# Optimization experiments

Hardware: AMD Instinct MI355X
Metric: run time of the kernel (lower is better)

Reference implementation:

```python
import jax, jax.numpy as jnp
import numpy as np

BIAS = 0.1  # init kwarg `bias`
B = 8192


def setup_inputs() -> dict:
    key = jax.random.key(0)
    k1, k2, k3 = jax.random.split(key, 3)
    predictions = jax.random.normal(k1, (B,), dtype=jnp.float32)
    correct_output = jax.random.normal(k2, (B,), dtype=jnp.float32)
    weight = jax.random.uniform(k3, (B,), dtype=jnp.float32)
    return {"predictions": predictions, "correct_output": correct_output, "weight": weight}


def reference(predictions, correct_output, weight):
    # pairwise diffs: [B, B], diff[m, n] = pred_m - pred_n
    diff = predictions[:, None] - predictions[None, :]
    gt_diff = correct_output[:, None] - correct_output[None, :]
    # r = +1 if pred_m > pred_n, -1 if pred_m < pred_n, else -sign(gt_m - gt_n)
    r = jnp.where(diff > 0, 1.0, jnp.where(diff < 0, -1.0, -jnp.sign(gt_diff)))
    # weighted by average pair weight
    r = r * (weight[:, None] + weight[None, :]) * 0.5
    loss = jnp.maximum(0.0, BIAS - r * diff)  # hinge per pair
    return jnp.sum(loss) / (B * B)
```

## Files before the change

### kernel.cpp

```cpp
#include <hip/hip_runtime.h>


#define BIAS_F 0.1f

typedef float v2f __attribute__((ext_vector_type(2)));

constexpr int TPB = 512;
constexpr int NPT = 8;
constexpr int NG  = NPT / 2;
constexpr int TN  = TPB * NPT;
constexpr int TM  = 32;

__global__ __launch_bounds__(TPB) void pair_loss_kernel(
    const float* __restrict__ pred,
    const float* __restrict__ weight,
    float* __restrict__ partial,
    int B)
{
    const int n_base = blockIdx.x * TN;
    const int m_base = blockIdx.y * TM;
    const int t = threadIdx.x;

    v2f pn2[NG], wn2[NG], mask2[NG];

    if (n_base + TN <= B) {
        const float4* p4 = reinterpret_cast<const float4*>(pred   + n_base) + 2 * t;
        const float4* w4 = reinterpret_cast<const float4*>(weight + n_base) + 2 * t;
        float4 pa = p4[0], pb = p4[1];
        float4 wa = w4[0], wb = w4[1];
        pn2[0] = (v2f){pa.x, pa.y}; pn2[1] = (v2f){pa.z, pa.w};
        pn2[2] = (v2f){pb.x, pb.y}; pn2[3] = (v2f){pb.z, pb.w};
        wn2[0] = (v2f){wa.x, wa.y} * 0.5f; wn2[1] = (v2f){wa.z, wa.w} * 0.5f;
        wn2[2] = (v2f){wb.x, wb.y} * 0.5f; wn2[3] = (v2f){wb.z, wb.w} * 0.5f;
        #pragma unroll
        for (int j = 0; j < NG; ++j) mask2[j] = (v2f){1.0f, 1.0f};
    } else {
        #pragma unroll
        for (int j = 0; j < NG; ++j) {
            #pragma unroll
            for (int e = 0; e < 2; ++e) {
                int n = n_base + 8 * t + 2 * j + e;
                bool ok = (n < B);
                int nc = ok ? n : 0;
                pn2[j][e]   = pred[nc];
                wn2[j][e]   = weight[nc] * 0.5f;
                mask2[j][e] = ok ? 1.0f : 0.0f;
            }
        }
    }

    v2f acc2[NG];
    #pragma unroll
    for (int j = 0; j < NG; ++j) acc2[j] = (v2f){0.0f, 0.0f};

    const v2f BIAS2 = (v2f){BIAS_F, BIAS_F};
    const int m_end = (m_base + TM <= B) ? TM : (B - m_base);

    #pragma unroll 4
    for (int i = 0; i < m_end; ++i) {
        const int m = m_base + i;
        const float pm  = pred[m];
        const float wmh = weight[m] * 0.5f;
        const v2f pm2 = (v2f){pm, pm};
        const v2f wm2 = (v2f){wmh, wmh};
        #pragma unroll
        for (int j = 0; j < NG; ++j) {
            v2f d  = pm2 - pn2[j];
            v2f w  = wm2 + wn2[j];
            v2f t1 = __builtin_elementwise_fma(-w, d, BIAS2);
            v2f t2 = __builtin_elementwise_fma( w, d, BIAS2);
            v2f h;
            h.x = __builtin_amdgcn_fmed3f(t1.x, t2.x, 0.0f);
            h.y = __builtin_amdgcn_fmed3f(t1.y, t2.y, 0.0f);
            acc2[j] += h;
        }
    }

    float s = 0.0f;
    #pragma unroll
    for (int j = 0; j < NG; ++j)
        s += mask2[j].x * acc2[j].x + mask2[j].y * acc2[j].y;

    #pragma unroll
    for (int off = 32; off > 0; off >>= 1)
        s += __shfl_down(s, off, 64);

    __shared__ float lds[TPB / 64];
    const int lane = t & 63, wid = t >> 6;
    if (lane == 0) lds[wid] = s;
    __syncthreads();
    if (t == 0) {
        float bs = 0.0f;
        #pragma unroll
        for (int w = 0; w < TPB / 64; ++w) bs += lds[w];
        partial[blockIdx.y * gridDim.x + blockIdx.x] = bs;
    }
}

__global__ __launch_bounds__(64) void reduce_kernel(
    const float* __restrict__ partial, int n, float* __restrict__ out, int B)
{
    double s = 0.0;
    for (int i = (int)threadIdx.x; i < n; i += 64) s += (double)partial[i];
    #pragma unroll
    for (int off = 32; off > 0; off >>= 1)
        s += __shfl_down(s, off, 64);
    if (threadIdx.x == 0)
        out[0] = (float)(s / ((double)B * (double)B));
}

extern "C" void kernel_launch(void* const* d_in, const int* in_sizes, int n_in,
                              void* d_out, int out_size, void* d_ws, size_t ws_size,
                              hipStream_t stream) {
    const float* pred   = (const float*)d_in[0];
    const float* weight = (const float*)d_in[2];
    float* out = (float*)d_out;
    const int B = in_sizes[0];

    const int tilesN = (B + TN - 1) / TN;
    const int tilesM = (B + TM - 1) / TM;
    float* partial = (float*)d_ws;

    dim3 grid(tilesN, tilesM);
    pair_loss_kernel<<<grid, TPB, 0, stream>>>(pred, weight, partial, B);
    reduce_kernel<<<1, 64, 0, stream>>>(partial, tilesN * tilesM, out, B);
}
```

Measured before the change: 18.02 us.

## Fuse final reduction into main kernel via fixed-point atomic last-block detection

Removes the separate reduce kernel. Each block now adds its partial sum as a fixed-point value packed with a completion counter into a single 64-bit atomic, and the last block writes the final result. Blocks are restructured to 1024 threads, each looping over all n tiles for its 32-row m tile, so the grid is one-dimensional. A memset launch replaces the reduce launch, and fixed-point quantization and a 48-bit range limit the precision of the sum.

```diff
diff --git a/kernel.cpp b/kernel.cpp
--- a/kernel.cpp
+++ b/kernel.cpp
@@ -2,85 +2,90 @@
 
 
 #define BIAS_F 0.1f
+#define FIX_SCALE 4194304.0
 
 typedef float v2f __attribute__((ext_vector_type(2)));
 
-constexpr int TPB = 512;
+constexpr int TPB = 1024;
 constexpr int NPT = 8;
 constexpr int NG  = NPT / 2;
-constexpr int TN  = TPB * NPT;
+constexpr int TNF = TPB * NPT;
 constexpr int TM  = 32;
 
 __global__ __launch_bounds__(TPB) void pair_loss_kernel(
     const float* __restrict__ pred,
     const float* __restrict__ weight,
-    float* __restrict__ partial,
-    int B)
+    unsigned long long* __restrict__ acc,
+    float* __restrict__ out,
+    int B, int nBlocks)
 {
-    const int n_base = blockIdx.x * TN;
-    const int m_base = blockIdx.y * TM;
+    const int m_base = blockIdx.x * TM;
     const int t = threadIdx.x;
 
-    v2f pn2[NG], wn2[NG], mask2[NG];
+    float s_thread = 0.0f;
+    const v2f BIAS2 = (v2f){BIAS_F, BIAS_F};
 
-    if (n_base + TN <= B) {
-        const float4* p4 = reinterpret_cast<const float4*>(pred   + n_base) + 2 * t;
-        const float4* w4 = reinterpret_cast<const float4*>(weight + n_base) + 2 * t;
-        float4 pa = p4[0], pb = p4[1];
-        float4 wa = w4[0], wb = w4[1];
-        pn2[0] = (v2f){pa.x, pa.y}; pn2[1] = (v2f){pa.z, pa.w};
-        pn2[2] = (v2f){pb.x, pb.y}; pn2[3] = (v2f){pb.z, pb.w};
-        wn2[0] = (v2f){wa.x, wa.y} * 0.5f; wn2[1] = (v2f){wa.z, wa.w} * 0.5f;
-        wn2[2] = (v2f){wb.x, wb.y} * 0.5f; wn2[3] = (v2f){wb.z, wb.w} * 0.5f;
-        #pragma unroll
-        for (int j = 0; j < NG; ++j) mask2[j] = (v2f){1.0f, 1.0f};
-    } else {
-        #pragma unroll
-        for (int j = 0; j < NG; ++j) {
+    for (int n_base = 0; n_base < B; n_base += TNF) {
+        v2f pn2[NG], wn2[NG], mask2[NG];
+        const int n_first = n_base + 8 * t;
+
+        if (n_base + TNF <= B) {
+            const float4* p4 = reinterpret_cast<const float4*>(pred   + n_base) + 2 * t;
+            const float4* w4 = reinterpret_cast<const float4*>(weight + n_base) + 2 * t;
+            float4 pa = p4[0], pb = p4[1];
+            float4 wa = w4[0], wb = w4[1];
+            pn2[0] = (v2f){pa.x, pa.y}; pn2[1] = (v2f){pa.z, pa.w};
+            pn2[2] = (v2f){pb.x, pb.y}; pn2[3] = (v2f){pb.z, pb.w};
+            wn2[0] = (v2f){wa.x, wa.y} * 0.5f; wn2[1] = (v2f){wa.z, wa.w} * 0.5f;
+            wn2[2] = (v2f){wb.x, wb.y} * 0.5f; wn2[3] = (v2f){wb.z, wb.w} * 0.5f;
             #pragma unroll
-            for (int e = 0; e < 2; ++e) {
-                int n = n_base + 8 * t + 2 * j + e;
-                bool ok = (n < B);
-                int nc = ok ? n : 0;
-                pn2[j][e]   = pred[nc];
-                wn2[j][e]   = weight[nc] * 0.5f;
-                mask2[j][e] = ok ? 1.0f : 0.0f;
+            for (int j = 0; j < NG; ++j) mask2[j] = (v2f){1.0f, 1.0f};
+        } else {
+            #pragma unroll
+            for (int j = 0; j < NG; ++j) {
+                #pragma unroll
+                for (int e = 0; e < 2; ++e) {
+                    int n = n_first + 2 * j + e;
+                    bool ok = (n < B);
+                    int nc = ok ? n : 0;
+                    pn2[j][e]   = pred[nc];
+                    wn2[j][e]   = weight[nc] * 0.5f;
+                    mask2[j][e] = ok ? 1.0f : 0.0f;
+                }
             }
         }
+
+        v2f acc2[NG];
+        #pragma unroll
+        for (int j = 0; j < NG; ++j) acc2[j] = (v2f){0.0f, 0.0f};
+
+        const int m_end = (m_base + TM <= B) ? TM : (B - m_base);
+        #pragma unroll 4
+        for (int i = 0; i < m_end; ++i) {
+            const int m = m_base + i;
+            const float pm  = pred[m];
+            const float wmh = weight[m] * 0.5f;
+            const v2f pm2 = (v2f){pm, pm};
+            const v2f wm2 = (v2f){wmh, wmh};
+            #pragma unroll
+            for (int j = 0; j < NG; ++j) {
+                v2f d  = pm2 - pn2[j];
+                v2f w  = wm2 + wn2[j];
+                v2f t1 = __builtin_elementwise_fma(-w, d, BIAS2);
+                v2f t2 = __builtin_elementwise_fma( w, d, BIAS2);
+                v2f h;
+                h.x = __builtin_amdgcn_fmed3f(t1.x, t2.x, 0.0f);
+                h.y = __builtin_amdgcn_fmed3f(t1.y, t2.y, 0.0f);
+                acc2[j] += h;
+            }
+        }
+
+        #pragma unroll
+        for (int j = 0; j < NG; ++j)
+            s_thread += mask2[j].x * acc2[j].x + mask2[j].y * acc2[j].y;
     }
 
-    v2f acc2[NG];
-    #pragma unroll
-    for (int j = 0; j < NG; ++j) acc2[j] = (v2f){0.0f, 0.0f};
-
-    const v2f BIAS2 = (v2f){BIAS_F, BIAS_F};
-    const int m_end = (m_base + TM <= B) ? TM : (B - m_base);
-
-    #pragma unroll 4
-    for (int i = 0; i < m_end; ++i) {
-        const int m = m_base + i;
-        const float pm  = pred[m];
-        const float wmh = weight[m] * 0.5f;
-        const v2f pm2 = (v2f){pm, pm};
-        const v2f wm2 = (v2f){wmh, wmh};
-        #pragma unroll
-        for (int j = 0; j < NG; ++j) {
-            v2f d  = pm2 - pn2[j];
-            v2f w  = wm2 + wn2[j];
-            v2f t1 = __builtin_elementwise_fma(-w, d, BIAS2);
-            v2f t2 = __builtin_elementwise_fma( w, d, BIAS2);
-            v2f h;
-            h.x = __builtin_amdgcn_fmed3f(t1.x, t2.x, 0.0f);
-            h.y = __builtin_amdgcn_fmed3f(t1.y, t2.y, 0.0f);
-            acc2[j] += h;
-        }
-    }
-
-    float s = 0.0f;
-    #pragma unroll
-    for (int j = 0; j < NG; ++j)
-        s += mask2[j].x * acc2[j].x + mask2[j].y * acc2[j].y;
-
+    float s = s_thread;
     #pragma unroll
     for (int off = 32; off > 0; off >>= 1)
         s += __shfl_down(s, off, 64);
@@ -89,24 +94,21 @@
     const int lane = t & 63, wid = t >> 6;
     if (lane == 0) lds[wid] = s;
     __syncthreads();
+
     if (t == 0) {
         float bs = 0.0f;
         #pragma unroll
         for (int w = 0; w < TPB / 64; ++w) bs += lds[w];
-        partial[blockIdx.y * gridDim.x + blockIdx.x] = bs;
+        unsigned long long fix =
+            (unsigned long long)llrint((double)bs * FIX_SCALE);
+        unsigned long long add = (1ULL << 48) | fix;
+        unsigned long long old = atomicAdd(acc, add);
+        if ((old >> 48) == (unsigned long long)(nBlocks - 1)) {
+            unsigned long long total_fix = (old & ((1ULL << 48) - 1)) + fix;
+            double total = (double)total_fix / FIX_SCALE;
+            out[0] = (float)(total / ((double)B * (double)B));
+        }
     }
-}
-
-__global__ __launch_bounds__(64) void reduce_kernel(
-    const float* __restrict__ partial, int n, float* __restrict__ out, int B)
-{
-    double s = 0.0;
-    for (int i = (int)threadIdx.x; i < n; i += 64) s += (double)partial[i];
-    #pragma unroll
-    for (int off = 32; off > 0; off >>= 1)
-        s += __shfl_down(s, off, 64);
-    if (threadIdx.x == 0)
-        out[0] = (float)(s / ((double)B * (double)B));
 }
 
 extern "C" void kernel_launch(void* const* d_in, const int* in_sizes, int n_in,
@@ -117,11 +119,9 @@
     float* out = (float*)d_out;
     const int B = in_sizes[0];
 
-    const int tilesN = (B + TN - 1) / TN;
-    const int tilesM = (B + TM - 1) / TM;
-    float* partial = (float*)d_ws;
+    unsigned long long* acc = (unsigned long long*)d_ws;
+    hipMemsetAsync(acc, 0, 8, stream);
 
-    dim3 grid(tilesN, tilesM);
-    pair_loss_kernel<<<grid, TPB, 0, stream>>>(pred, weight, partial, B);
-    reduce_kernel<<<1, 64, 0, stream>>>(partial, tilesN * tilesM, out, B);
+    const int nBlocks = (B + TM - 1) / TM;
+    pair_loss_kernel<<<nBlocks, TPB, 0, stream>>>(pred, weight, acc, out, B, nBlocks);
 }
```

Result: slower. 21.60 us (+19.9%).
